# Optimization experiments

Measured on AMD Instinct MI355X. Metric: run time of the kernel, lower is better.

## Reference

```python
import jax, jax.numpy as jnp
import numpy as np


def setup_inputs() -> dict:
    key = jax.random.key(0)
    k1, k2 = jax.random.split(key)
    B, C, H, W = 32, 256, 64, 64
    data = jax.random.normal(k1, (B, C, H, W), dtype=jnp.float32)
    offset = jax.random.normal(k2, (B, 2, H, W), dtype=jnp.float32)
    trans_std = jnp.float32(0.005)  # learned scalar Parameter
    return {"data": data, "offset": offset, "trans_std": trans_std}


def reference(data, offset, trans_std):
    """Offset-driven bilinear interpolation sampling + global average pooling.

    data:   [B, C, H, W]
    offset: [B, 2, H, W]  (dy, dx) displacement field, scaled by trans_std
    Returns pooled features [B, C].
    """
    B, C, H, W = data.shape
    ts = jnp.clip(trans_std, 0.001, 0.01)  # forward clamps trans_std to [0.001, 0.01]

    # sampling coordinates: base grid + scaled offsets (offsets normalized by H/W)
    ii = jnp.arange(H, dtype=data.dtype)[:, None]   # [H,1]
    jj = jnp.arange(W, dtype=data.dtype)[None, :]   # [1,W]
    y = jnp.clip(ii + ts * offset[:, 0] * H, 0.0, H - 1)  # [B,H,W]
    x = jnp.clip(jj + ts * offset[:, 1] * W, 0.0, W - 1)  # [B,H,W]

    y0 = jnp.clip(jnp.floor(y).astype(jnp.int32), 0, H - 2)
    x0 = jnp.clip(jnp.floor(x).astype(jnp.int32), 0, W - 2)
    y1 = y0 + 1
    x1 = x0 + 1
    wy = y - y0.astype(data.dtype)  # [B,H,W] in [0,1]
    wx = x - x0.astype(data.dtype)

    def sample_one(d, yy0, yy1, xx0, xx1):
        # d: [C,H,W]; index maps: [H,W] -> gathered [C,H,W]
        v00 = d[:, yy0, xx0]
        v01 = d[:, yy0, xx1]
        v10 = d[:, yy1, xx0]
        v11 = d[:, yy1, xx1]
        return v00, v01, v10, v11

    v00, v01, v10, v11 = jax.vmap(sample_one)(data, y0, y1, x0, x1)  # each [B,C,H,W]

    wy_ = wy[:, None]  # broadcast over channels -> [B,1,H,W]
    wx_ = wx[:, None]
    sampled = ((1 - wy_) * (1 - wx_) * v00 + (1 - wy_) * wx_ * v01
               + wy_ * (1 - wx_) * v10 + wy_ * wx_ * v11)  # [B,C,H,W]

    # pooling: global average over spatial locations -> [B,C]
    return jnp.mean(sampled, axis=(2, 3))
```

## Files before the change

### kernel.cpp

```cpp
#include <hip/hip_runtime.h>

#define BATCH 32
#define CHAN  256
#define HGT   64
#define WID   64
#define HW    4096
#define CPB   16

__global__ __launch_bounds__(1024, 4) void fused_bilinear_pool(
        const float* __restrict__ data,
        const float* __restrict__ offset,
        const float* __restrict__ ts_ptr,
        float* __restrict__ out)
{
    const int blk  = blockIdx.x;
    const int b    = blk >> 4;
    const int g    = blk & 15;
    const int tid  = threadIdx.x;
    const int w    = tid >> 6;
    const int lane = tid & 63;

    __shared__ float acc[HW];

    acc[tid]        = 0.0f;
    acc[tid + 1024] = 0.0f;
    acc[tid + 2048] = 0.0f;
    acc[tid + 3072] = 0.0f;
    __syncthreads();

    const float* off_y = offset + (size_t)b * 2 * HW;
    const float* off_x = off_y + HW;
    const float4 dy4 = *reinterpret_cast<const float4*>(off_y + tid * 4);
    const float4 dx4 = *reinterpret_cast<const float4*>(off_x + tid * 4);

    const float* plane = data + ((size_t)(b * CHAN + g * CPB + w)) * HW;
    float4 d[16];
    #pragma unroll
    for (int s = 0; s < 16; ++s)
        d[s] = *reinterpret_cast<const float4*>(plane + s * 256 + lane * 4);

    float ts = ts_ptr[0];
    ts = fminf(fmaxf(ts, 0.001f), 0.01f);

    {
        const int i  = tid >> 4;
        const int j0 = (tid << 2) & 63;
        const float dys[4] = {dy4.x, dy4.y, dy4.z, dy4.w};
        const float dxs[4] = {dx4.x, dx4.y, dx4.z, dx4.w};
        #pragma unroll
        for (int e = 0; e < 4; ++e) {
            float y = fminf(fmaxf((float)i        + ts * dys[e] * 64.0f, 0.0f), 63.0f);
            float x = fminf(fmaxf((float)(j0 + e) + ts * dxs[e] * 64.0f, 0.0f), 63.0f);
            int y0 = (int)floorf(y); y0 = min(max(y0, 0), HGT - 2);
            int x0 = (int)floorf(x); x0 = min(max(x0, 0), WID - 2);
            const float wy = y - (float)y0;
            const float wx = x - (float)x0;
            const int base = (y0 << 6) + x0;
            atomicAdd(&acc[base],           (1.0f - wy) * (1.0f - wx));
            atomicAdd(&acc[base + 1],       (1.0f - wy) * wx);
            atomicAdd(&acc[base + WID],     wy * (1.0f - wx));
            atomicAdd(&acc[base + WID + 1], wy * wx);
        }
    }
    __syncthreads();

    float a0 = 0.0f, a1 = 0.0f, a2 = 0.0f, a3 = 0.0f;
    #pragma unroll
    for (int s = 0; s < 16; ++s) {
        const float4 av =
            *reinterpret_cast<const float4*>(acc + s * 256 + lane * 4);
        if ((s & 3) == 0) {
            a0 = fmaf(av.x, d[s].x, a0); a0 = fmaf(av.y, d[s].y, a0);
            a0 = fmaf(av.z, d[s].z, a0); a0 = fmaf(av.w, d[s].w, a0);
        } else if ((s & 3) == 1) {
            a1 = fmaf(av.x, d[s].x, a1); a1 = fmaf(av.y, d[s].y, a1);
            a1 = fmaf(av.z, d[s].z, a1); a1 = fmaf(av.w, d[s].w, a1);
        } else if ((s & 3) == 2) {
            a2 = fmaf(av.x, d[s].x, a2); a2 = fmaf(av.y, d[s].y, a2);
            a2 = fmaf(av.z, d[s].z, a2); a2 = fmaf(av.w, d[s].w, a2);
        } else {
            a3 = fmaf(av.x, d[s].x, a3); a3 = fmaf(av.y, d[s].y, a3);
            a3 = fmaf(av.z, d[s].z, a3); a3 = fmaf(av.w, d[s].w, a3);
        }
    }
    float sum = (a0 + a1) + (a2 + a3);

    #pragma unroll
    for (int off = 32; off > 0; off >>= 1)
        sum += __shfl_down(sum, off, 64);

    if (lane == 0)
        out[(b << 8) + g * CPB + w] = sum * (1.0f / (float)HW);
}

extern "C" void kernel_launch(void* const* d_in, const int* in_sizes, int n_in,
                              void* d_out, int out_size, void* d_ws, size_t ws_size,
                              hipStream_t stream) {
    const float* data   = (const float*)d_in[0];
    const float* offset = (const float*)d_in[1];
    const float* ts     = (const float*)d_in[2];

    float* out = (float*)d_out;
    (void)d_ws; (void)ws_size;

    fused_bilinear_pool<<<BATCH * CPB, 1024, 0, stream>>>(data, offset, ts, out);
}
```

Baseline: 204.1 us.

## Process two channel planes per wave with inline-asm double-buffered global loads

Each block now handles 32 channels instead of 16, which halves the block count and the per-block weight-map (atomic splat) setup cost that used to be repeated for every channel group. Data loads are issued with inline global_load_dwordx4 into two register buffers and waited on with explicit vmcnt counts, so loading the second plane overlaps the LDS dot product of the first. The loads also now start after the atomic phase instead of before it. This risks lower occupancy and less latency hiding, since there are only 256 blocks and the launch-bounds occupancy hint is gone, and the hand-written waitcnt has to stay correct.

New measurement: 214.9 us. 5.3% more time.

```diff
diff --git a/kernel.cpp b/kernel.cpp
--- a/kernel.cpp
+++ b/kernel.cpp
@@ -1,21 +1,58 @@
 #include <hip/hip_runtime.h>
+#include <stdint.h>
 
 #define BATCH 32
 #define CHAN  256
 #define HGT   64
 #define WID   64
 #define HW    4096
-#define CPB   16
+#define GPB   8
+#define CPB   32
 
-__global__ __launch_bounds__(1024, 4) void fused_bilinear_pool(
+typedef float v4f __attribute__((ext_vector_type(4)));
+
+#define GLOAD8(B0,B1,B2,B3,B4,B5,B6,B7, P0, P1)                       \
+    asm volatile(                                                      \
+        "global_load_dwordx4 %0, %8, off\n\t"                          \
+        "global_load_dwordx4 %1, %8, off offset:1024\n\t"              \
+        "global_load_dwordx4 %2, %8, off offset:2048\n\t"              \
+        "global_load_dwordx4 %3, %8, off offset:3072\n\t"              \
+        "global_load_dwordx4 %4, %9, off\n\t"                          \
+        "global_load_dwordx4 %5, %9, off offset:1024\n\t"              \
+        "global_load_dwordx4 %6, %9, off offset:2048\n\t"              \
+        "global_load_dwordx4 %7, %9, off offset:3072"                  \
+        : "=&v"(B0), "=&v"(B1), "=&v"(B2), "=&v"(B3),                  \
+          "=&v"(B4), "=&v"(B5), "=&v"(B6), "=&v"(B7)                   \
+        : "v"(P0), "v"(P1)                                             \
+        : "memory")
+
+#define WAITVM(N)                                                      \
+    asm volatile("s_waitcnt vmcnt(" #N ")" ::: "memory");              \
+    __builtin_amdgcn_sched_barrier(0)
+
+#define FMA4(S, AV, DV)                                                \
+    S = fmaf((AV).x, (DV).x, S); S = fmaf((AV).y, (DV).y, S);          \
+    S = fmaf((AV).z, (DV).z, S); S = fmaf((AV).w, (DV).w, S)
+
+#define DRAIN8(B0,B1,B2,B3,B4,B5,B6,B7, HP, S0,S1,S2,S3)               \
+    { const float4 a0_ = *reinterpret_cast<const float4*>((HP) + 0*256); FMA4(S0, a0_, B0); \
+      const float4 a1_ = *reinterpret_cast<const float4*>((HP) + 1*256); FMA4(S1, a1_, B1); \
+      const float4 a2_ = *reinterpret_cast<const float4*>((HP) + 2*256); FMA4(S2, a2_, B2); \
+      const float4 a3_ = *reinterpret_cast<const float4*>((HP) + 3*256); FMA4(S3, a3_, B3); \
+      const float4 a4_ = *reinterpret_cast<const float4*>((HP) + 4*256); FMA4(S0, a4_, B4); \
+      const float4 a5_ = *reinterpret_cast<const float4*>((HP) + 5*256); FMA4(S1, a5_, B5); \
+      const float4 a6_ = *reinterpret_cast<const float4*>((HP) + 6*256); FMA4(S2, a6_, B6); \
+      const float4 a7_ = *reinterpret_cast<const float4*>((HP) + 7*256); FMA4(S3, a7_, B7); }
+
+__global__ __launch_bounds__(1024) void fused_bilinear_pool(
         const float* __restrict__ data,
         const float* __restrict__ offset,
         const float* __restrict__ ts_ptr,
         float* __restrict__ out)
 {
     const int blk  = blockIdx.x;
-    const int b    = blk >> 4;
-    const int g    = blk & 15;
+    const int b    = blk >> 3;
+    const int g    = blk & 7;
     const int tid  = threadIdx.x;
     const int w    = tid >> 6;
     const int lane = tid & 63;
@@ -32,12 +69,6 @@
     const float* off_x = off_y + HW;
     const float4 dy4 = *reinterpret_cast<const float4*>(off_y + tid * 4);
     const float4 dx4 = *reinterpret_cast<const float4*>(off_x + tid * 4);
-
-    const float* plane = data + ((size_t)(b * CHAN + g * CPB + w)) * HW;
-    float4 d[16];
-    #pragma unroll
-    for (int s = 0; s < 16; ++s)
-        d[s] = *reinterpret_cast<const float4*>(plane + s * 256 + lane * 4);
 
     float ts = ts_ptr[0];
     ts = fminf(fmaxf(ts, 0.001f), 0.01f);
@@ -64,33 +95,50 @@
     }
     __syncthreads();
 
-    float a0 = 0.0f, a1 = 0.0f, a2 = 0.0f, a3 = 0.0f;
-    #pragma unroll
-    for (int s = 0; s < 16; ++s) {
-        const float4 av =
-            *reinterpret_cast<const float4*>(acc + s * 256 + lane * 4);
-        if ((s & 3) == 0) {
-            a0 = fmaf(av.x, d[s].x, a0); a0 = fmaf(av.y, d[s].y, a0);
-            a0 = fmaf(av.z, d[s].z, a0); a0 = fmaf(av.w, d[s].w, a0);
-        } else if ((s & 3) == 1) {
-            a1 = fmaf(av.x, d[s].x, a1); a1 = fmaf(av.y, d[s].y, a1);
-            a1 = fmaf(av.z, d[s].z, a1); a1 = fmaf(av.w, d[s].w, a1);
-        } else if ((s & 3) == 2) {
-            a2 = fmaf(av.x, d[s].x, a2); a2 = fmaf(av.y, d[s].y, a2);
-            a2 = fmaf(av.z, d[s].z, a2); a2 = fmaf(av.w, d[s].w, a2);
-        } else {
-            a3 = fmaf(av.x, d[s].x, a3); a3 = fmaf(av.y, d[s].y, a3);
-            a3 = fmaf(av.z, d[s].z, a3); a3 = fmaf(av.w, d[s].w, a3);
-        }
-    }
-    float sum = (a0 + a1) + (a2 + a3);
+    const int c0 = g * CPB;
+    const float* p0 = data + ((size_t)b * CHAN + c0 + w) * HW + lane * 4;
+    const float* p1 = p0 + 16 * HW;
+
+    const float* hp0 = acc + lane * 4;
+    const float* hp1 = acc + 2048 + lane * 4;
+
+    v4f A0,A1,A2,A3,A4,A5,A6,A7;
+    v4f B0,B1,B2,B3,B4,B5,B6,B7;
+
+    GLOAD8(A0,A1,A2,A3,A4,A5,A6,A7, p0,        p0 + 1024);
+    GLOAD8(B0,B1,B2,B3,B4,B5,B6,B7, p0 + 2048, p0 + 3072);
+
+    float s0=0.f,s1=0.f,s2=0.f,s3=0.f;
+    float t0=0.f,t1=0.f,t2=0.f,t3=0.f;
+
+    WAITVM(8);
+    DRAIN8(A0,A1,A2,A3,A4,A5,A6,A7, hp0, s0,s1,s2,s3);
+    GLOAD8(A0,A1,A2,A3,A4,A5,A6,A7, p1,        p1 + 1024);
+
+    WAITVM(8);
+    DRAIN8(B0,B1,B2,B3,B4,B5,B6,B7, hp1, s0,s1,s2,s3);
+    GLOAD8(B0,B1,B2,B3,B4,B5,B6,B7, p1 + 2048, p1 + 3072);
+
+    WAITVM(8);
+    DRAIN8(A0,A1,A2,A3,A4,A5,A6,A7, hp0, t0,t1,t2,t3);
+
+    WAITVM(0);
+    DRAIN8(B0,B1,B2,B3,B4,B5,B6,B7, hp1, t0,t1,t2,t3);
+
+    float sum0 = (s0 + s1) + (s2 + s3);
+    float sum1 = (t0 + t1) + (t2 + t3);
 
     #pragma unroll
-    for (int off = 32; off > 0; off >>= 1)
-        sum += __shfl_down(sum, off, 64);
+    for (int off = 32; off > 0; off >>= 1) {
+        sum0 += __shfl_down(sum0, off, 64);
+        sum1 += __shfl_down(sum1, off, 64);
+    }
 
-    if (lane == 0)
-        out[(b << 8) + g * CPB + w] = sum * (1.0f / (float)HW);
+    if (lane == 0) {
+        const float s = 1.0f / (float)HW;
+        out[(b << 8) + c0 + w]      = sum0 * s;
+        out[(b << 8) + c0 + w + 16] = sum1 * s;
+    }
 }
 
 extern "C" void kernel_launch(void* const* d_in, const int* in_sizes, int n_in,
@@ -103,5 +151,5 @@
     float* out = (float*)d_out;
     (void)d_ws; (void)ws_size;
 
-    fused_bilinear_pool<<<BATCH * CPB, 1024, 0, stream>>>(data, offset, ts, out);
+    fused_bilinear_pool<<<BATCH * GPB, 1024, 0, stream>>>(data, offset, ts, out);
 }
```
